# Kernel optimization log

Hardware: AMD Instinct MI355X
Metric: run time of the kernel (lower is better)

Reference implementation:

```python
import jax, jax.numpy as jnp
import numpy as np

HEADS = 8
DIM_HEAD = 64
SCALE = DIM_HEAD ** -0.5


def setup_inputs() -> dict:
    key = jax.random.key(0)
    ks = jax.random.split(key, 8)
    B, Nq, Nk, D = 4, 1024, 2048, 512
    inner = HEADS * DIM_HEAD  # 512
    x = jax.random.normal(ks[0], (B, Nq, D), dtype=jnp.float32)
    context = jax.random.normal(ks[1], (B, Nk, D), dtype=jnp.float32)
    bias = jax.random.normal(ks[2], (B, Nq, Nk), dtype=jnp.float32)
    s = D ** -0.5
    Wq = jax.random.normal(ks[3], (inner, D), dtype=jnp.float32) * s
    Wk = jax.random.normal(ks[4], (inner, D), dtype=jnp.float32) * s
    Wv = jax.random.normal(ks[5], (inner, D), dtype=jnp.float32) * s
    Wo = jax.random.normal(ks[6], (D, inner), dtype=jnp.float32) * s
    bo = jnp.zeros((D,), dtype=jnp.float32)
    return {"x": x, "context": context, "bias": bias,
            "Wq": Wq, "Wk": Wk, "Wv": Wv, "Wo": Wo, "bo": bo}


def reference(x, context, bias, Wq, Wk, Wv, Wo, bo):
    B, Nq, _ = x.shape
    # torch Linear: y = x @ W.T ; reshape (h d) -> b h n d
    q = (x @ Wq.T).reshape(B, Nq, HEADS, DIM_HEAD).transpose(0, 2, 1, 3)
    k = (context @ Wk.T).reshape(B, -1, HEADS, DIM_HEAD).transpose(0, 2, 1, 3)
    v = (context @ Wv.T).reshape(B, -1, HEADS, DIM_HEAD).transpose(0, 2, 1, 3)
    # explicit-score fallback path (bias supplied)
    scores = jnp.einsum('bhqd,bhkd->bhqk', q, k) * SCALE
    scores = scores + bias[:, None, :, :]  # 3D bias -> (B,1,Nq,Nk)
    attn = jax.nn.softmax(scores, axis=-1)
    out = jnp.einsum('bhqk,bhkd->bhqd', attn, v)
    out = out.transpose(0, 2, 1, 3).reshape(B, Nq, HEADS * DIM_HEAD)
    return out @ Wo.T + bo
```

## Files before the change

kernel.cpp:

```cpp
#include <hip/hip_runtime.h>

#define H 8
#define DH 64
#define NQ 1024
#define NK 2048
#define DIN 512
#define B 4
#define KSPLIT 2
#define KRANGE (NK / KSPLIT)
#define KTILES (KRANGE / 64)
#define BHNQ (B * H * NQ)

typedef __bf16 bf16;
typedef __bf16 bf16x8 __attribute__((ext_vector_type(8)));
typedef __bf16 bf16x4 __attribute__((ext_vector_type(4)));
typedef float floatx4 __attribute__((ext_vector_type(4)));

__device__ inline void gload16(const void* g, void* l) {
  __builtin_amdgcn_global_load_lds(
      (const __attribute__((address_space(1))) void*)g,
      (__attribute__((address_space(3))) void*)l, 16, 0, 0);
}

__device__ inline float fexp2(float x) {
#if __has_builtin(__builtin_amdgcn_exp2f)
  return __builtin_amdgcn_exp2f(x);
#else
  return exp2f(x);
#endif
}

__global__ void cvt_all(const float* __restrict__ x, const float* __restrict__ ctx,
                        const float* __restrict__ wq, const float* __restrict__ wk,
                        const float* __restrict__ wv, const float* __restrict__ wo,
                        bf16* xb, bf16* cb, bf16* wqb, bf16* wkb, bf16* wvb, bf16* wob) {
  long i = ((long)blockIdx.x * 256 + threadIdx.x) * 4;
  const float* s; bf16* d; long o;
  if (i < 2097152)      { s = x;   d = xb;  o = i; }
  else if (i < 6291456) { s = ctx; d = cb;  o = i - 2097152; }
  else if (i < 6553600) { s = wq;  d = wqb; o = i - 6291456; }
  else if (i < 6815744) { s = wk;  d = wkb; o = i - 6553600; }
  else if (i < 7077888) { s = wv;  d = wvb; o = i - 6815744; }
  else                  { s = wo;  d = wob; o = i - 7077888; }
  float4 f = *(const float4*)(s + o);
  bf16x4 v = { (bf16)f.x, (bf16)f.y, (bf16)f.z, (bf16)f.w };
  *(bf16x4*)(d + o) = v;
}

__global__ __launch_bounds__(256) void gemm_qkv(
    const bf16* __restrict__ xb, const bf16* __restrict__ cb,
    const bf16* __restrict__ wqb, const bf16* __restrict__ wkb, const bf16* __restrict__ wvb,
    bf16* __restrict__ qb, bf16* __restrict__ kb, bf16* __restrict__ vtb) {
  const bool qmode = (blockIdx.z == 0);
  if (qmode && blockIdx.y >= 64) return;

  __shared__ bf16 Al[2][64 * 32];
  __shared__ bf16 Bk[2][128 * 32];
  __shared__ bf16 Bv[2][128 * 32];
  const int t = threadIdx.x;
  const int lane = t & 63, w = t >> 6;
  const int ln = lane & 15, quad = lane >> 4;
  const int wm = (w >> 1) * 32, wn = (w & 1) * 64;
  const int rowBase = blockIdx.y * 64;
  const int colBase = blockIdx.x * 128;

  const bf16* A  = qmode ? xb : cb;
  const bf16* W1 = qmode ? wqb : wkb;

  floatx4 accK[2][4] = {};
  floatx4 accV[2][4] = {};
  const int rA = t >> 2, oA = (t & 3) * 8;
  const int c0 = t, c1 = t + 256;
  const int rB0 = c0 >> 2, oB0 = (c0 & 3) * 8;
  const int rB1 = c1 >> 2, oB1 = (c1 & 3) * 8;
  const bf16* Ab  = A + (size_t)rowBase * DIN;
  const bf16* Wb1 = W1 + (size_t)colBase * DIN;
  const bf16* Wbv = wvb + (size_t)colBase * DIN;

  gload16(Ab + (size_t)rA * DIN + oA, &Al[0][t * 8]);
  gload16(Wb1 + (size_t)rB0 * DIN + oB0, &Bk[0][c0 * 8]);
  gload16(Wb1 + (size_t)rB1 * DIN + oB1, &Bk[0][c1 * 8]);
  if (!qmode) {
    gload16(Wbv + (size_t)rB0 * DIN + oB0, &Bv[0][c0 * 8]);
    gload16(Wbv + (size_t)rB1 * DIN + oB1, &Bv[0][c1 * 8]);
  }
  __syncthreads();

  for (int k0 = 0; k0 < DIN; k0 += 32) {
    const int cur = (k0 >> 5) & 1, nxt = cur ^ 1;
    if (k0 + 32 < DIN) {
      gload16(Ab + (size_t)rA * DIN + k0 + 32 + oA, &Al[nxt][t * 8]);
      gload16(Wb1 + (size_t)rB0 * DIN + k0 + 32 + oB0, &Bk[nxt][c0 * 8]);
      gload16(Wb1 + (size_t)rB1 * DIN + k0 + 32 + oB1, &Bk[nxt][c1 * 8]);
      if (!qmode) {
        gload16(Wbv + (size_t)rB0 * DIN + k0 + 32 + oB0, &Bv[nxt][c0 * 8]);
        gload16(Wbv + (size_t)rB1 * DIN + k0 + 32 + oB1, &Bv[nxt][c1 * 8]);
      }
    }
    bf16x8 af[2], bK[4];
#pragma unroll
    for (int i = 0; i < 2; i++)
      af[i] = *(const bf16x8*)&Al[cur][(wm + i * 16 + ln) * 32 + quad * 8];
#pragma unroll
    for (int j = 0; j < 4; j++)
      bK[j] = *(const bf16x8*)&Bk[cur][(wn + j * 16 + ln) * 32 + quad * 8];
#pragma unroll
    for (int i = 0; i < 2; i++)
#pragma unroll
      for (int j = 0; j < 4; j++)
        accK[i][j] = __builtin_amdgcn_mfma_f32_16x16x32_bf16(af[i], bK[j], accK[i][j], 0, 0, 0);
    if (!qmode) {
      bf16x8 bV[4];
#pragma unroll
      for (int j = 0; j < 4; j++)
        bV[j] = *(const bf16x8*)&Bv[cur][(wn + j * 16 + ln) * 32 + quad * 8];
#pragma unroll
      for (int i = 0; i < 2; i++)
#pragma unroll
        for (int j = 0; j < 4; j++)
          accV[i][j] = __builtin_amdgcn_mfma_f32_16x16x32_bf16(bV[j], af[i], accV[i][j], 0, 0, 0);
    }
    __syncthreads();
  }

  if (qmode) {
#pragma unroll
    for (int i = 0; i < 2; i++)
#pragma unroll
      for (int j = 0; j < 4; j++)
#pragma unroll
        for (int r = 0; r < 4; r++) {
          const int m = rowBase + wm + i * 16 + quad * 4 + r;
          const int n = colBase + wn + j * 16 + ln;
          const float v = accK[i][j][r] * 0.125f;
          const int bb = m >> 10, tok = m & 1023;
          const int hh = n >> 6, d = n & 63;
          qb[((((size_t)(bb * H + hh)) << 10) + tok) * DH + d] = (bf16)v;
        }
  } else {
#pragma unroll
    for (int i = 0; i < 2; i++)
#pragma unroll
      for (int j = 0; j < 4; j++)
#pragma unroll
        for (int r = 0; r < 4; r++) {
          const int m = rowBase + wm + i * 16 + quad * 4 + r;
          const int n = colBase + wn + j * 16 + ln;
          const int bb = m >> 11, tok = m & 2047;
          const int hh = n >> 6, d = n & 63;
          kb[((((size_t)(bb * H + hh)) << 11) + tok) * DH + d] = (bf16)accK[i][j][r];
          const int dg = colBase + wn + j * 16 + quad * 4 + r;
          const int mv = rowBase + wm + i * 16 + ln;
          const int bbv = mv >> 11, tokv = mv & 2047;
          const int hhv = dg >> 6, dv = dg & 63;
          vtb[((((size_t)(bbv * H + hhv)) * DH + dv) << 11) + tokv] = (bf16)accV[i][j][r];
        }
  }
}

__global__ __launch_bounds__(256) void attn_fwd(
    const bf16* __restrict__ q, const bf16* __restrict__ k,
    const bf16* __restrict__ vt, const float* __restrict__ bias,
    float* __restrict__ op0, float* __restrict__ op1, float* __restrict__ lpart) {
  __shared__ bf16 KL[64 * 64];
  __shared__ bf16 VL[64 * 64];
  __shared__ __attribute__((aligned(16))) bf16 Pl[4][2][16][64];
  const int tid = threadIdx.x;
  const int lane = tid & 63, w = tid >> 6;
  const int ln = lane & 15, quad = lane >> 4;
  const int hh = blockIdx.y;
  const int b = blockIdx.z >> 1, ks = blockIdx.z & 1;
  const int q0 = blockIdx.x * 128;
  const int k0 = ks * KRANGE;
  const size_t bh = (size_t)b * H + hh;
  const bf16* qp = q + bh * NQ * DH;
  const bf16* kp = k + bh * NK * DH;
  const bf16* vp = vt + bh * DH * NK;
  const float* bp0 = bias + ((size_t)b * NQ + q0 + w * 32 + ln) * NK + k0 + quad * 4;
  const float* bp1 = bp0 + (size_t)16 * NK;

  bf16x8 qf[2][2];
#pragma unroll
  for (int s = 0; s < 2; s++)
#pragma unroll
    for (int kc = 0; kc < 2; kc++)
      qf[s][kc] = *(const bf16x8*)(qp + (size_t)(q0 + w * 32 + s * 16 + ln) * DH + kc * 32 + quad * 8);

  floatx4 o[2][4] = {};
  floatx4 lac[2] = {};
  const bf16x8 ones = {(bf16)1.f, (bf16)1.f, (bf16)1.f, (bf16)1.f,
                       (bf16)1.f, (bf16)1.f, (bf16)1.f, (bf16)1.f};
  constexpr float L2E = 1.44269504f;
  constexpr float OFF = 34.6246810f;

  for (int tt = 0; tt < KTILES; tt++) {
    const int nk0 = k0 + tt * 64;
#pragma unroll
    for (int s = 0; s < 2; s++) {
      const int i = s * 256 + tid;
      const int sr = i >> 3, sc = (i & 7) ^ (sr & 7);
      gload16(kp + (size_t)(nk0 + sr) * DH + sc * 8, &KL[i * 8]);
      gload16(vp + (size_t)sr * NK + nk0 + sc * 8, &VL[i * 8]);
    }
    floatx4 s4[2][4];
#pragma unroll
    for (int j = 0; j < 4; j++) {
      s4[0][j] = *(const floatx4*)(bp0 + tt * 64 + j * 16);
      s4[1][j] = *(const floatx4*)(bp1 + tt * 64 + j * 16);
    }
    __syncthreads();

#pragma unroll
    for (int j = 0; j < 4; j++)
#pragma unroll
      for (int kc = 0; kc < 2; kc++) {
        const int kr = j * 16 + ln;
        bf16x8 kf = *(const bf16x8*)&KL[kr * 64 + (((kc * 4 + quad) ^ (kr & 7)) * 8)];
        s4[0][j] = __builtin_amdgcn_mfma_f32_16x16x32_bf16(kf, qf[0][kc], s4[0][j], 0, 0, 0);
        s4[1][j] = __builtin_amdgcn_mfma_f32_16x16x32_bf16(kf, qf[1][kc], s4[1][j], 0, 0, 0);
      }

#pragma unroll
    for (int s = 0; s < 2; s++)
#pragma unroll
      for (int j = 0; j < 4; j++) {
        const float e0 = fexp2(fmaf(s4[s][j][0], L2E, -OFF));
        const float e1 = fexp2(fmaf(s4[s][j][1], L2E, -OFF));
        const float e2 = fexp2(fmaf(s4[s][j][2], L2E, -OFF));
        const float e3 = fexp2(fmaf(s4[s][j][3], L2E, -OFF));
        bf16x4 pv4 = {(bf16)e0, (bf16)e1, (bf16)e2, (bf16)e3};
        const int tok = (j * 16 + quad * 4) ^ ((ln & 7) << 3);
        *(bf16x4*)&Pl[w][s][ln][tok] = pv4;
      }
    asm volatile("s_waitcnt lgkmcnt(0)" ::: "memory");

    bf16x8 pt[2][2];
#pragma unroll
    for (int s = 0; s < 2; s++)
#pragma unroll
      for (int kc = 0; kc < 2; kc++) {
        const int tok = (kc * 32 + quad * 8) ^ ((ln & 7) << 3);
        pt[s][kc] = *(const bf16x8*)&Pl[w][s][ln][tok];
      }

#pragma unroll
    for (int s = 0; s < 2; s++)
#pragma unroll
      for (int kc = 0; kc < 2; kc++)
        lac[s] = __builtin_amdgcn_mfma_f32_16x16x32_bf16(ones, pt[s][kc], lac[s], 0, 0, 0);

#pragma unroll
    for (int jn = 0; jn < 4; jn++)
#pragma unroll
      for (int kc = 0; kc < 2; kc++) {
        const int vr = jn * 16 + ln;
        bf16x8 vf = *(const bf16x8*)&VL[vr * 64 + (((kc * 4 + quad) ^ (vr & 7)) * 8)];
        o[0][jn] = __builtin_amdgcn_mfma_f32_16x16x32_bf16(vf, pt[0][kc], o[0][jn], 0, 0, 0);
        o[1][jn] = __builtin_amdgcn_mfma_f32_16x16x32_bf16(vf, pt[1][kc], o[1][jn], 0, 0, 0);
      }
    __syncthreads();
  }

#pragma unroll
  for (int s = 0; s < 2; s++) {
    float* op = (ks ? op1 : op0) +
                ((size_t)b * NQ + q0 + w * 32 + s * 16 + ln) * DIN + hh * 64 + quad * 4;
#pragma unroll
    for (int jn = 0; jn < 4; jn++)
      *(floatx4*)(op + jn * 16) = o[s][jn];
    if (quad == 0)
      lpart[((size_t)ks * B * H + b * H + hh) * NQ + q0 + w * 32 + s * 16 + ln] = lac[s][0];
  }
}

__global__ __launch_bounds__(256) void gemm_out(
    const float* __restrict__ op0, const float* __restrict__ op1,
    const float* __restrict__ lp, const bf16* __restrict__ W,
    float* __restrict__ outf, const float* __restrict__ bo) {
  __shared__ bf16 Al[2][32 * 32];
  __shared__ bf16 Bl[2][128 * 32];
  const int t = threadIdx.x;
  const int lane = t & 63, w = t >> 6;
  const int ln = lane & 15, quad = lane >> 4;
  const int wm = (w >> 1) * 16, wn = (w & 1) * 64;
  const int rowBase = blockIdx.y * 32;
  const int colBase = blockIdx.x * 128;

  floatx4 acc[4] = {};
  const int rA = t >> 2, oA = (t & 3) * 8;
  const int c0 = t, c1 = t + 256;
  const int rB0 = c0 >> 2, oB0 = (c0 & 3) * 8;
  const int rB1 = c1 >> 2, oB1 = (c1 & 3) * 8;
  const int m0 = rowBase + rA;
  const bf16* Wb = W + (size_t)colBase * DIN;

  float linv0[8];
  if (t < 128) {
#pragma unroll
    for (int h = 0; h < 8; h++) {
      const int i0 = ((m0 >> 10) * H + h) * NQ + (m0 & 1023);
      linv0[h] = 1.0f / (lp[i0] + lp[BHNQ + i0]);
    }
  }

#define STAGE_A(K0V, BUF)                                                      \
  if (t < 128) {                                                               \
    const float sA = linv0[(K0V) >> 6];                                        \
    const float* pa0 = op0 + (size_t)m0 * DIN + (K0V) + oA;                    \
    const float* pa1 = op1 + (size_t)m0 * DIN + (K0V) + oA;                    \
    float4 xa = *(const float4*)pa0, xb2 = *(const float4*)(pa0 + 4);          \
    float4 ya = *(const float4*)pa1, yb = *(const float4*)(pa1 + 4);           \
    bf16x8 v0 = {(bf16)((xa.x + ya.x) * sA), (bf16)((xa.y + ya.y) * sA),       \
                 (bf16)((xa.z + ya.z) * sA), (bf16)((xa.w + ya.w) * sA),       \
                 (bf16)((xb2.x + yb.x) * sA), (bf16)((xb2.y + yb.y) * sA),     \
                 (bf16)((xb2.z + yb.z) * sA), (bf16)((xb2.w + yb.w) * sA)};    \
    *(bf16x8*)&Al[BUF][t * 8] = v0;                                            \
  }

  STAGE_A(0, 0);
  gload16(Wb + (size_t)rB0 * DIN + oB0, &Bl[0][c0 * 8]);
  gload16(Wb + (size_t)rB1 * DIN + oB1, &Bl[0][c1 * 8]);
  __syncthreads();

#pragma unroll
  for (int kk = 0; kk < 16; kk++) {
    const int cur = kk & 1, nxt = cur ^ 1;
    if (kk < 15) {
      const int k1 = (kk + 1) * 32;
      STAGE_A(k1, nxt);
      gload16(Wb + (size_t)rB0 * DIN + k1 + oB0, &Bl[nxt][c0 * 8]);
      gload16(Wb + (size_t)rB1 * DIN + k1 + oB1, &Bl[nxt][c1 * 8]);
    }
    bf16x8 af, bfr[4];
    af = *(const bf16x8*)&Al[cur][(wm + ln) * 32 + quad * 8];
#pragma unroll
    for (int j = 0; j < 4; j++)
      bfr[j] = *(const bf16x8*)&Bl[cur][(wn + j * 16 + ln) * 32 + quad * 8];
#pragma unroll
    for (int j = 0; j < 4; j++)
      acc[j] = __builtin_amdgcn_mfma_f32_16x16x32_bf16(af, bfr[j], acc[j], 0, 0, 0);
    __syncthreads();
  }
#undef STAGE_A

#pragma unroll
  for (int j = 0; j < 4; j++)
#pragma unroll
    for (int r = 0; r < 4; r++) {
      const int m = rowBase + wm + quad * 4 + r;
      const int n = colBase + wn + j * 16 + ln;
      outf[(size_t)m * DIN + n] = acc[j][r] + bo[n];
    }
}

extern "C" void kernel_launch(void* const* d_in, const int* in_sizes, int n_in,
                              void* d_out, int out_size, void* d_ws, size_t ws_size,
                              hipStream_t stream) {
  const float* x    = (const float*)d_in[0];
  const float* ctx  = (const float*)d_in[1];
  const float* bias = (const float*)d_in[2];
  const float* Wq   = (const float*)d_in[3];
  const float* Wk   = (const float*)d_in[4];
  const float* Wv   = (const float*)d_in[5];
  const float* Wo   = (const float*)d_in[6];
  const float* bo   = (const float*)d_in[7];
  float* out = (float*)d_out;

  char* p = (char*)d_ws;
  bf16* xb   = (bf16*)(p + 0);
  bf16* cb   = (bf16*)(p + 4194304);
  bf16* wqb  = (bf16*)(p + 12582912);
  bf16* wkb  = (bf16*)(p + 13107200);
  bf16* wvb  = (bf16*)(p + 13631488);
  bf16* wob  = (bf16*)(p + 14155776);
  bf16* qb   = (bf16*)(p + 14680064);
  bf16* kb   = (bf16*)(p + 18874368);
  bf16* vtb  = (bf16*)(p + 27262976);
  float* op1 = (float*)(p + 35651584);
  float* lpart = (float*)(p + 44040192);
  float* op0 = (float*)cb;

  cvt_all<<<7168, 256, 0, stream>>>(x, ctx, Wq, Wk, Wv, Wo, xb, cb, wqb, wkb, wvb, wob);
  gemm_qkv<<<dim3(4, 128, 2), 256, 0, stream>>>(xb, cb, wqb, wkb, wvb, qb, kb, vtb);
  attn_fwd<<<dim3(NQ / 128, H, B * KSPLIT), 256, 0, stream>>>(qb, kb, vtb, bias, op0, op1, lpart);
  gemm_out<<<dim3(4, 128), 256, 0, stream>>>(op0, op1, lpart, wob, out, bo);
}
```

Measured before the change: 185.1 us.

## Double-buffer K/V tiles in LDS and prefetch bias one tile ahead

The attention kernel's K/V shared-memory tiles become double-buffered. The loop is unrolled by two, so the global-to-LDS loads for the next tile and the bias loads into registers are issued before the current tile's MFMA and softmax work. Explicit vmcnt waits and raw s_barrier calls with sched_barrier fences replace __syncthreads, so the next tile's transfers overlap current compute. The cost is doubled K/V LDS usage and extra bias registers, which may reduce occupancy.

```diff
diff --git a/kernel.cpp b/kernel.cpp
--- a/kernel.cpp
+++ b/kernel.cpp
@@ -162,8 +162,8 @@
     const bf16* __restrict__ q, const bf16* __restrict__ k,
     const bf16* __restrict__ vt, const float* __restrict__ bias,
     float* __restrict__ op0, float* __restrict__ op1, float* __restrict__ lpart) {
-  __shared__ bf16 KL[64 * 64];
-  __shared__ bf16 VL[64 * 64];
+  __shared__ bf16 KL[2][64 * 64];
+  __shared__ bf16 VL[2][64 * 64];
   __shared__ __attribute__((aligned(16))) bf16 Pl[4][2][16][64];
   const int tid = threadIdx.x;
   const int lane = tid & 63, w = tid >> 6;
@@ -193,73 +193,111 @@
   constexpr float L2E = 1.44269504f;
   constexpr float OFF = 34.6246810f;
 
-  for (int tt = 0; tt < KTILES; tt++) {
-    const int nk0 = k0 + tt * 64;
-#pragma unroll
-    for (int s = 0; s < 2; s++) {
-      const int i = s * 256 + tid;
-      const int sr = i >> 3, sc = (i & 7) ^ (sr & 7);
-      gload16(kp + (size_t)(nk0 + sr) * DH + sc * 8, &KL[i * 8]);
-      gload16(vp + (size_t)sr * NK + nk0 + sc * 8, &VL[i * 8]);
-    }
-    floatx4 s4[2][4];
-#pragma unroll
-    for (int j = 0; j < 4; j++) {
-      s4[0][j] = *(const floatx4*)(bp0 + tt * 64 + j * 16);
-      s4[1][j] = *(const floatx4*)(bp1 + tt * 64 + j * 16);
-    }
-    __syncthreads();
-
-#pragma unroll
-    for (int j = 0; j < 4; j++)
-#pragma unroll
-      for (int kc = 0; kc < 2; kc++) {
-        const int kr = j * 16 + ln;
-        bf16x8 kf = *(const bf16x8*)&KL[kr * 64 + (((kc * 4 + quad) ^ (kr & 7)) * 8)];
-        s4[0][j] = __builtin_amdgcn_mfma_f32_16x16x32_bf16(kf, qf[0][kc], s4[0][j], 0, 0, 0);
-        s4[1][j] = __builtin_amdgcn_mfma_f32_16x16x32_bf16(kf, qf[1][kc], s4[1][j], 0, 0, 0);
-      }
-
-#pragma unroll
-    for (int s = 0; s < 2; s++)
-#pragma unroll
-      for (int j = 0; j < 4; j++) {
-        const float e0 = fexp2(fmaf(s4[s][j][0], L2E, -OFF));
-        const float e1 = fexp2(fmaf(s4[s][j][1], L2E, -OFF));
-        const float e2 = fexp2(fmaf(s4[s][j][2], L2E, -OFF));
-        const float e3 = fexp2(fmaf(s4[s][j][3], L2E, -OFF));
-        bf16x4 pv4 = {(bf16)e0, (bf16)e1, (bf16)e2, (bf16)e3};
-        const int tok = (j * 16 + quad * 4) ^ ((ln & 7) << 3);
-        *(bf16x4*)&Pl[w][s][ln][tok] = pv4;
-      }
-    asm volatile("s_waitcnt lgkmcnt(0)" ::: "memory");
-
-    bf16x8 pt[2][2];
-#pragma unroll
-    for (int s = 0; s < 2; s++)
-#pragma unroll
-      for (int kc = 0; kc < 2; kc++) {
-        const int tok = (kc * 32 + quad * 8) ^ ((ln & 7) << 3);
-        pt[s][kc] = *(const bf16x8*)&Pl[w][s][ln][tok];
-      }
-
-#pragma unroll
-    for (int s = 0; s < 2; s++)
-#pragma unroll
-      for (int kc = 0; kc < 2; kc++)
-        lac[s] = __builtin_amdgcn_mfma_f32_16x16x32_bf16(ones, pt[s][kc], lac[s], 0, 0, 0);
-
-#pragma unroll
-    for (int jn = 0; jn < 4; jn++)
-#pragma unroll
-      for (int kc = 0; kc < 2; kc++) {
-        const int vr = jn * 16 + ln;
-        bf16x8 vf = *(const bf16x8*)&VL[vr * 64 + (((kc * 4 + quad) ^ (vr & 7)) * 8)];
-        o[0][jn] = __builtin_amdgcn_mfma_f32_16x16x32_bf16(vf, pt[0][kc], o[0][jn], 0, 0, 0);
-        o[1][jn] = __builtin_amdgcn_mfma_f32_16x16x32_bf16(vf, pt[1][kc], o[1][jn], 0, 0, 0);
-      }
-    __syncthreads();
-  }
+  floatx4 bcA[2][4], bcB[2][4];
+
+#define STAGE(NB, TT)                                                          \
+  {                                                                            \
+    const int nk0_ = k0 + (TT) * 64;                                           \
+    _Pragma("unroll")                                                          \
+    for (int s_ = 0; s_ < 2; s_++) {                                           \
+      const int i_ = s_ * 256 + tid;                                           \
+      const int sr_ = i_ >> 3, sc_ = (i_ & 7) ^ (sr_ & 7);                     \
+      gload16(kp + (size_t)(nk0_ + sr_) * DH + sc_ * 8, &KL[NB][i_ * 8]);      \
+      gload16(vp + (size_t)sr_ * NK + nk0_ + sc_ * 8, &VL[NB][i_ * 8]);        \
+    }                                                                          \
+  }
+
+#define LOADB(BC, TT)                                                          \
+  {                                                                            \
+    _Pragma("unroll")                                                          \
+    for (int j_ = 0; j_ < 4; j_++) {                                           \
+      BC[0][j_] = *(const floatx4*)(bp0 + (TT) * 64 + j_ * 16);                \
+      BC[1][j_] = *(const floatx4*)(bp1 + (TT) * 64 + j_ * 16);                \
+    }                                                                          \
+  }
+
+#define COMPUTE(CUR, BC)                                                              \
+  {                                                                                   \
+    floatx4 s4[2][4];                                                                 \
+    _Pragma("unroll")                                                                 \
+    for (int s_ = 0; s_ < 2; s_++)                                                    \
+      _Pragma("unroll")                                                               \
+      for (int j_ = 0; j_ < 4; j_++)                                                  \
+        s4[s_][j_] = BC[s_][j_];                                                      \
+    _Pragma("unroll")                                                                 \
+    for (int j_ = 0; j_ < 4; j_++)                                                    \
+      _Pragma("unroll")                                                               \
+      for (int kc_ = 0; kc_ < 2; kc_++) {                                             \
+        const int kr_ = j_ * 16 + ln;                                                 \
+        bf16x8 kf = *(const bf16x8*)&KL[CUR][kr_ * 64 + (((kc_ * 4 + quad) ^ (kr_ & 7)) * 8)]; \
+        s4[0][j_] = __builtin_amdgcn_mfma_f32_16x16x32_bf16(kf, qf[0][kc_], s4[0][j_], 0, 0, 0); \
+        s4[1][j_] = __builtin_amdgcn_mfma_f32_16x16x32_bf16(kf, qf[1][kc_], s4[1][j_], 0, 0, 0); \
+      }                                                                               \
+    _Pragma("unroll")                                                                 \
+    for (int s_ = 0; s_ < 2; s_++)                                                    \
+      _Pragma("unroll")                                                               \
+      for (int j_ = 0; j_ < 4; j_++) {                                                \
+        const float e0 = fexp2(fmaf(s4[s_][j_][0], L2E, -OFF));                       \
+        const float e1 = fexp2(fmaf(s4[s_][j_][1], L2E, -OFF));                       \
+        const float e2 = fexp2(fmaf(s4[s_][j_][2], L2E, -OFF));                       \
+        const float e3 = fexp2(fmaf(s4[s_][j_][3], L2E, -OFF));                       \
+        bf16x4 pv4 = {(bf16)e0, (bf16)e1, (bf16)e2, (bf16)e3};                        \
+        const int tok_ = (j_ * 16 + quad * 4) ^ ((ln & 7) << 3);                      \
+        *(bf16x4*)&Pl[w][s_][ln][tok_] = pv4;                                         \
+      }                                                                               \
+    asm volatile("s_waitcnt lgkmcnt(0)" ::: "memory");                                \
+    bf16x8 pt[2][2];                                                                  \
+    _Pragma("unroll")                                                                 \
+    for (int s_ = 0; s_ < 2; s_++)                                                    \
+      _Pragma("unroll")                                                               \
+      for (int kc_ = 0; kc_ < 2; kc_++) {                                             \
+        const int tok_ = (kc_ * 32 + quad * 8) ^ ((ln & 7) << 3);                     \
+        pt[s_][kc_] = *(const bf16x8*)&Pl[w][s_][ln][tok_];                           \
+      }                                                                               \
+    _Pragma("unroll")                                                                 \
+    for (int s_ = 0; s_ < 2; s_++)                                                    \
+      _Pragma("unroll")                                                               \
+      for (int kc_ = 0; kc_ < 2; kc_++)                                               \
+        lac[s_] = __builtin_amdgcn_mfma_f32_16x16x32_bf16(ones, pt[s_][kc_], lac[s_], 0, 0, 0); \
+    _Pragma("unroll")                                                                 \
+    for (int jn_ = 0; jn_ < 4; jn_++)                                                 \
+      _Pragma("unroll")                                                               \
+      for (int kc_ = 0; kc_ < 2; kc_++) {                                             \
+        const int vr_ = jn_ * 16 + ln;                                                \
+        bf16x8 vf = *(const bf16x8*)&VL[CUR][vr_ * 64 + (((kc_ * 4 + quad) ^ (vr_ & 7)) * 8)]; \
+        o[0][jn_] = __builtin_amdgcn_mfma_f32_16x16x32_bf16(vf, pt[0][kc_], o[0][jn_], 0, 0, 0); \
+        o[1][jn_] = __builtin_amdgcn_mfma_f32_16x16x32_bf16(vf, pt[1][kc_], o[1][jn_], 0, 0, 0); \
+      }                                                                               \
+  }
+
+  STAGE(0, 0);
+  LOADB(bcA, 0);
+
+  for (int tt = 0; tt < KTILES; tt += 2) {
+    STAGE(1, tt + 1);
+    asm volatile("s_waitcnt vmcnt(4)" ::: "memory");
+    __builtin_amdgcn_sched_barrier(0);
+    __builtin_amdgcn_s_barrier();
+    __builtin_amdgcn_sched_barrier(0);
+    LOADB(bcB, tt + 1);
+    COMPUTE(0, bcA);
+    __builtin_amdgcn_s_barrier();
+    if (tt + 2 < KTILES) {
+      STAGE(0, tt + 2);
+      asm volatile("s_waitcnt vmcnt(4)" ::: "memory");
+    } else {
+      asm volatile("s_waitcnt vmcnt(0)" ::: "memory");
+    }
+    __builtin_amdgcn_sched_barrier(0);
+    __builtin_amdgcn_s_barrier();
+    __builtin_amdgcn_sched_barrier(0);
+    if (tt + 2 < KTILES) LOADB(bcA, tt + 2);
+    COMPUTE(1, bcB);
+    __builtin_amdgcn_s_barrier();
+  }
+#undef STAGE
+#undef LOADB
+#undef COMPUTE
 
 #pragma unroll
   for (int s = 0; s < 2; s++) {
```

New measurement: 188.4 us. No clear change (+1.8%).

## Split attention keys four ways with 512-thread blocks and MFMA priority hints

Applied to the files above, without the earlier changes.

Doubles the key-range split from two to four partial outputs and doubles the block to 512 threads covering 256 queries. Each K/V tile is now shared by eight waves, and every thread issues a single async load per tile. s_setprio is raised around the MFMA sections. The output GEMM now sums four partial outputs and four row-sum parts, which adds global write and read traffic and workspace.

```diff
diff --git a/kernel.cpp b/kernel.cpp
--- a/kernel.cpp
+++ b/kernel.cpp
@@ -6,7 +6,7 @@
 #define NK 2048
 #define DIN 512
 #define B 4
-#define KSPLIT 2
+#define KSPLIT 4
 #define KRANGE (NK / KSPLIT)
 #define KTILES (KRANGE / 64)
 #define BHNQ (B * H * NQ)
@@ -158,19 +158,20 @@
   }
 }
 
-__global__ __launch_bounds__(256) void attn_fwd(
+__global__ __launch_bounds__(512) void attn_fwd(
     const bf16* __restrict__ q, const bf16* __restrict__ k,
     const bf16* __restrict__ vt, const float* __restrict__ bias,
-    float* __restrict__ op0, float* __restrict__ op1, float* __restrict__ lpart) {
+    float* __restrict__ op0, float* __restrict__ op1,
+    float* __restrict__ op2, float* __restrict__ op3, float* __restrict__ lpart) {
   __shared__ bf16 KL[64 * 64];
   __shared__ bf16 VL[64 * 64];
-  __shared__ __attribute__((aligned(16))) bf16 Pl[4][2][16][64];
+  __shared__ __attribute__((aligned(16))) bf16 Pl[8][2][16][64];
   const int tid = threadIdx.x;
   const int lane = tid & 63, w = tid >> 6;
   const int ln = lane & 15, quad = lane >> 4;
   const int hh = blockIdx.y;
-  const int b = blockIdx.z >> 1, ks = blockIdx.z & 1;
-  const int q0 = blockIdx.x * 128;
+  const int b = blockIdx.z >> 2, ks = blockIdx.z & 3;
+  const int q0 = blockIdx.x * 256;
   const int k0 = ks * KRANGE;
   const size_t bh = (size_t)b * H + hh;
   const bf16* qp = q + bh * NQ * DH;
@@ -195,9 +196,8 @@
 
   for (int tt = 0; tt < KTILES; tt++) {
     const int nk0 = k0 + tt * 64;
-#pragma unroll
-    for (int s = 0; s < 2; s++) {
-      const int i = s * 256 + tid;
+    {
+      const int i = tid;
       const int sr = i >> 3, sc = (i & 7) ^ (sr & 7);
       gload16(kp + (size_t)(nk0 + sr) * DH + sc * 8, &KL[i * 8]);
       gload16(vp + (size_t)sr * NK + nk0 + sc * 8, &VL[i * 8]);
@@ -210,6 +210,7 @@
     }
     __syncthreads();
 
+    __builtin_amdgcn_s_setprio(1);
 #pragma unroll
     for (int j = 0; j < 4; j++)
 #pragma unroll
@@ -219,6 +220,7 @@
         s4[0][j] = __builtin_amdgcn_mfma_f32_16x16x32_bf16(kf, qf[0][kc], s4[0][j], 0, 0, 0);
         s4[1][j] = __builtin_amdgcn_mfma_f32_16x16x32_bf16(kf, qf[1][kc], s4[1][j], 0, 0, 0);
       }
+    __builtin_amdgcn_s_setprio(0);
 
 #pragma unroll
     for (int s = 0; s < 2; s++)
@@ -243,6 +245,7 @@
         pt[s][kc] = *(const bf16x8*)&Pl[w][s][ln][tok];
       }
 
+    __builtin_amdgcn_s_setprio(1);
 #pragma unroll
     for (int s = 0; s < 2; s++)
 #pragma unroll
@@ -258,12 +261,14 @@
         o[0][jn] = __builtin_amdgcn_mfma_f32_16x16x32_bf16(vf, pt[0][kc], o[0][jn], 0, 0, 0);
         o[1][jn] = __builtin_amdgcn_mfma_f32_16x16x32_bf16(vf, pt[1][kc], o[1][jn], 0, 0, 0);
       }
+    __builtin_amdgcn_s_setprio(0);
     __syncthreads();
   }
 
+  float* opsel = (ks == 0) ? op0 : ((ks == 1) ? op1 : ((ks == 2) ? op2 : op3));
 #pragma unroll
   for (int s = 0; s < 2; s++) {
-    float* op = (ks ? op1 : op0) +
+    float* op = opsel +
                 ((size_t)b * NQ + q0 + w * 32 + s * 16 + ln) * DIN + hh * 64 + quad * 4;
 #pragma unroll
     for (int jn = 0; jn < 4; jn++)
@@ -275,6 +280,7 @@
 
 __global__ __launch_bounds__(256) void gemm_out(
     const float* __restrict__ op0, const float* __restrict__ op1,
+    const float* __restrict__ op2, const float* __restrict__ op3,
     const float* __restrict__ lp, const bf16* __restrict__ W,
     float* __restrict__ outf, const float* __restrict__ bo) {
   __shared__ bf16 Al[2][32 * 32];
@@ -299,21 +305,26 @@
 #pragma unroll
     for (int h = 0; h < 8; h++) {
       const int i0 = ((m0 >> 10) * H + h) * NQ + (m0 & 1023);
-      linv0[h] = 1.0f / (lp[i0] + lp[BHNQ + i0]);
+      linv0[h] = 1.0f / (lp[i0] + lp[BHNQ + i0] + lp[2 * BHNQ + i0] + lp[3 * BHNQ + i0]);
     }
   }
 
 #define STAGE_A(K0V, BUF)                                                      \
   if (t < 128) {                                                               \
     const float sA = linv0[(K0V) >> 6];                                        \
-    const float* pa0 = op0 + (size_t)m0 * DIN + (K0V) + oA;                    \
-    const float* pa1 = op1 + (size_t)m0 * DIN + (K0V) + oA;                    \
-    float4 xa = *(const float4*)pa0, xb2 = *(const float4*)(pa0 + 4);          \
-    float4 ya = *(const float4*)pa1, yb = *(const float4*)(pa1 + 4);           \
-    bf16x8 v0 = {(bf16)((xa.x + ya.x) * sA), (bf16)((xa.y + ya.y) * sA),       \
-                 (bf16)((xa.z + ya.z) * sA), (bf16)((xa.w + ya.w) * sA),       \
-                 (bf16)((xb2.x + yb.x) * sA), (bf16)((xb2.y + yb.y) * sA),     \
-                 (bf16)((xb2.z + yb.z) * sA), (bf16)((xb2.w + yb.w) * sA)};    \
+    const size_t off = (size_t)m0 * DIN + (K0V) + oA;                          \
+    float4 a0 = *(const float4*)(op0 + off), a1 = *(const float4*)(op0 + off + 4); \
+    float4 b0 = *(const float4*)(op1 + off), b1 = *(const float4*)(op1 + off + 4); \
+    float4 c0v = *(const float4*)(op2 + off), c1v = *(const float4*)(op2 + off + 4); \
+    float4 d0 = *(const float4*)(op3 + off), d1 = *(const float4*)(op3 + off + 4); \
+    bf16x8 v0 = {(bf16)((a0.x + b0.x + c0v.x + d0.x) * sA),                    \
+                 (bf16)((a0.y + b0.y + c0v.y + d0.y) * sA),                    \
+                 (bf16)((a0.z + b0.z + c0v.z + d0.z) * sA),                    \
+                 (bf16)((a0.w + b0.w + c0v.w + d0.w) * sA),                    \
+                 (bf16)((a1.x + b1.x + c1v.x + d1.x) * sA),                    \
+                 (bf16)((a1.y + b1.y + c1v.y + d1.y) * sA),                    \
+                 (bf16)((a1.z + b1.z + c1v.z + d1.z) * sA),                    \
+                 (bf16)((a1.w + b1.w + c1v.w + d1.w) * sA)};                   \
     *(bf16x8*)&Al[BUF][t * 8] = v0;                                            \
   }
 
@@ -377,11 +388,13 @@
   bf16* kb   = (bf16*)(p + 18874368);
   bf16* vtb  = (bf16*)(p + 27262976);
   float* op1 = (float*)(p + 35651584);
-  float* lpart = (float*)(p + 44040192);
+  float* op2 = (float*)(p + 44040192);
+  float* op3 = (float*)(p + 52428800);
+  float* lpart = (float*)(p + 60817408);
   float* op0 = (float*)cb;
 
   cvt_all<<<7168, 256, 0, stream>>>(x, ctx, Wq, Wk, Wv, Wo, xb, cb, wqb, wkb, wvb, wob);
   gemm_qkv<<<dim3(4, 128, 2), 256, 0, stream>>>(xb, cb, wqb, wkb, wvb, qb, kb, vtb);
-  attn_fwd<<<dim3(NQ / 128, H, B * KSPLIT), 256, 0, stream>>>(qb, kb, vtb, bias, op0, op1, lpart);
-  gemm_out<<<dim3(4, 128), 256, 0, stream>>>(op0, op1, lpart, wob, out, bo);
-}
+  attn_fwd<<<dim3(NQ / 256, H, B * KSPLIT), 512, 0, stream>>>(qb, kb, vtb, bias, op0, op1, op2, op3, lpart);
+  gemm_out<<<dim3(4, 128), 256, 0, stream>>>(op0, op1, op2, op3, lpart, wob, out, bo);
+}
```

New measurement: 188.7 us. About the same (+2.0%).
